# Kernel tuning notes

Measured on AMD Instinct MI355X. Metric: run time of the kernel, lower is better.

The kernel has to match this reference:

```python
import jax, jax.numpy as jnp
import numpy as np

H = 16   # num_heads
A = 64   # attn_size
D = 1024 # dims
NEG = -1000000000.0


def setup_inputs() -> dict:
    key = jax.random.key(0)
    k1, k2, k3, k4 = jax.random.split(key, 4)
    B, S = 2, 2048
    qs = jax.random.normal(k1, (B, S, D), dtype=jnp.float32)
    mask = jax.random.randint(k2, (B, S), 0, 2, dtype=jnp.int32)
    Wqkv = jax.random.normal(k3, (D, 3 * H * A), dtype=jnp.float32) * (1.0 / np.sqrt(D))
    Wout = jax.random.normal(k4, (H * A, D), dtype=jnp.float32) * (1.0 / np.sqrt(H * A))
    bout = jnp.zeros((D,), dtype=jnp.float32)
    return {"qs": qs, "mask": mask, "Wqkv": Wqkv, "Wout": Wout, "bout": bout}


def reference(qs, mask, Wqkv, Wout, bout):
    B, S, _ = qs.shape
    qkv = qs @ Wqkv                              # [B,S,3*H*A]
    qkv = qkv.reshape(B, S, 3 * H, A)            # split axis=2 in thirds (TF layout)
    q = jnp.transpose(qkv[:, :, 0:H, :], (0, 2, 1, 3))        # [B,H,S,A]
    k = jnp.transpose(qkv[:, :, H:2 * H, :], (0, 2, 1, 3))    # [B,H,S,A]
    v = jnp.transpose(qkv[:, :, 2 * H:3 * H, :], (0, 2, 1, 3))# [B,H,S,A]
    scores = jnp.einsum('bhqa,bhka->bhqk', q, k) / jnp.sqrt(jnp.float32(A))
    m = mask[:, None, None, :]                   # [B,1,1,S] broadcast over heads, queries
    scores = jnp.where(m == 0, NEG, scores)
    probs = jax.nn.softmax(scores, axis=-1)      # dropout_prob=0 / inference -> identity
    ctx = jnp.einsum('bhqk,bhka->bhqa', probs, v)  # [B,H,S,A]
    ctx = jnp.transpose(ctx, (0, 2, 1, 3)).reshape(B, S, H * A)
    return ctx @ Wout + bout
```

## Files before the change

### kernel.cpp

```cpp
#include <hip/hip_runtime.h>
#include <stdint.h>


typedef unsigned short u16;
typedef uint32_t u32;
typedef u16   u16x4  __attribute__((ext_vector_type(4)));
typedef u16   u16x8  __attribute__((ext_vector_type(8)));
typedef __bf16 bf16x8 __attribute__((ext_vector_type(8)));
typedef float f32x4  __attribute__((ext_vector_type(4)));

#define DEV __device__ __forceinline__

DEV u16 cvt_bf(float f) {
    return __builtin_bit_cast(u16, (__bf16)f);
}

DEV void async16(const void* g, void* l) {
    __builtin_amdgcn_global_load_lds(
        reinterpret_cast<const uint32_t __attribute__((address_space(1)))*>(
            reinterpret_cast<uintptr_t>(g)),
        reinterpret_cast<uint32_t __attribute__((address_space(3)))*>(
            reinterpret_cast<uintptr_t>(l)),
        16, 0, 0);
}

DEV f32x4 mfma16(bf16x8 a, bf16x8 b, f32x4 c) {
    return __builtin_amdgcn_mfma_f32_16x16x32_bf16(a, b, c, 0, 0, 0);
}


__global__ void k_prep(const float* __restrict__ qs, u16* __restrict__ qs_bf,
                       const int* __restrict__ m, float* __restrict__ bias) {
    int bid = blockIdx.x;
    if (bid < 4096) {
        int i = (bid * 256 + threadIdx.x) * 4;
        float4 v = *reinterpret_cast<const float4*>(qs + i);
        u16x4 o = { cvt_bf(v.x), cvt_bf(v.y), cvt_bf(v.z), cvt_bf(v.w) };
        *reinterpret_cast<u16x4*>(qs_bf + i) = o;
    } else {
        int i = (bid - 4096) * 256 + threadIdx.x;
        bias[i] = m[i] ? 0.0f : -1.0e9f;
    }
}

__global__ void k_tconv(const float* __restrict__ Wqkv, u16* __restrict__ WqkvT,
                        const float* __restrict__ Wout, u16* __restrict__ WoutT) {
    __shared__ float t[32][33];
    int bid = blockIdx.x;
    const float* src; u16* dst; int R, C, bx, by;
    if (bid < 3072) { src = Wqkv; dst = WqkvT; R = 1024; C = 3072; bx = bid % 96; by = bid / 96; }
    else { bid -= 3072; src = Wout; dst = WoutT; R = 1024; C = 1024; bx = bid % 32; by = bid / 32; }
    int c0 = bx * 32, r0 = by * 32;
    int tx = threadIdx.x & 31, ty = threadIdx.x >> 5;
#pragma unroll
    for (int i = 0; i < 4; ++i)
        t[ty + 8 * i][tx] = src[(size_t)(r0 + ty + 8 * i) * C + c0 + tx];
    __syncthreads();
#pragma unroll
    for (int i = 0; i < 4; ++i)
        dst[(size_t)(c0 + ty + 8 * i) * R + r0 + tx] = cvt_bf(t[tx][ty + 8 * i]);
}


template <int BM, bool OUT_BF16, bool HAS_BIAS>
__global__ __launch_bounds__(512, 4) void k_gemm(
    const u16* __restrict__ A, const u16* __restrict__ Bt,
    void* __restrict__ Cv, const float* __restrict__ bias,
    int M, int N, int K)
{
    constexpr int MT = BM / 32;
    __shared__ __attribute__((aligned(16))) u16 As[2][BM * 32];
    __shared__ __attribute__((aligned(16))) u16 Bs[2][128 * 32];

    const int tid = threadIdx.x, wave = tid >> 6, lane = tid & 63;
    const int lh = lane & 15, lg = lane >> 4;
    const int nbn = N >> 7;

    const int nwg = gridDim.x;
    const int q8 = nwg >> 3, r8 = nwg & 7;
    const int xcd = blockIdx.x & 7, li = blockIdx.x >> 3;
    const int wg = (xcd < r8 ? xcd * (q8 + 1) : r8 * (q8 + 1) + (xcd - r8) * q8) + li;

    const int m0 = (wg / nbn) * BM, n0 = (wg % nbn) * 128;
    const int wm = wave >> 2, wn = wave & 3;
    const int nk = K >> 5;

    const int srow = tid >> 2, scc = tid & 3;
    const int ssc = scc ^ (srow & 3);

    auto stage = [&](int buf, int kt) {
        if (tid < BM * 4)
            async16(A + (size_t)(m0 + srow) * K + kt * 32 + ssc * 8, &As[buf][tid * 8]);
        async16(Bt + (size_t)(n0 + srow) * K + kt * 32 + ssc * 8, &Bs[buf][tid * 8]);
    };

    f32x4 acc[MT][2] = {};
    stage(0, 0);
    for (int kt = 0; kt < nk; ++kt) {
        __syncthreads();
        if (kt + 1 < nk) stage((kt + 1) & 1, kt + 1);
        const int buf = kt & 1;
        bf16x8 af[MT], bf_[2];
#pragma unroll
        for (int mt = 0; mt < MT; ++mt) {
            int row = wm * (BM / 2) + mt * 16 + lh;
            int off = row * 32 + ((lg ^ (row & 3)) * 8);
            af[mt] = __builtin_bit_cast(bf16x8,
                     *reinterpret_cast<const u16x8*>(&As[buf][off]));
        }
#pragma unroll
        for (int nt = 0; nt < 2; ++nt) {
            int row = wn * 32 + nt * 16 + lh;
            int off = row * 32 + ((lg ^ (row & 3)) * 8);
            bf_[nt] = __builtin_bit_cast(bf16x8,
                      *reinterpret_cast<const u16x8*>(&Bs[buf][off]));
        }
        __builtin_amdgcn_s_setprio(1);
#pragma unroll
        for (int mt = 0; mt < MT; ++mt)
#pragma unroll
            for (int nt = 0; nt < 2; ++nt)
                acc[mt][nt] = mfma16(af[mt], bf_[nt], acc[mt][nt]);
        __builtin_amdgcn_s_setprio(0);
        __syncthreads();
    }

#pragma unroll
    for (int mt = 0; mt < MT; ++mt)
#pragma unroll
        for (int nt = 0; nt < 2; ++nt) {
            int col = n0 + wn * 32 + nt * 16 + lh;
#pragma unroll
            for (int r = 0; r < 4; ++r) {
                int row = m0 + wm * (BM / 2) + mt * 16 + 4 * lg + r;
                float v = acc[mt][nt][r];
                if (HAS_BIAS) v += bias[col];
                if (OUT_BF16) ((u16*)Cv)[(size_t)row * N + col] = cvt_bf(v);
                else          ((float*)Cv)[(size_t)row * N + col] = v;
            }
        }
}


__global__ __launch_bounds__(512, 4) void k_attn(
    const u16* __restrict__ qkv, const float* __restrict__ biasg, u16* __restrict__ ctx)
{
    __shared__ __attribute__((aligned(16))) u16 Ks[2][64 * 64];
    __shared__ __attribute__((aligned(16))) u16 Vt[2][64 * 72];
    __shared__ __attribute__((aligned(16))) u16 Ps[8 * 16 * 72];

    const int tid = threadIdx.x, wave = tid >> 6, lane = tid & 63;
    const int lh = lane & 15, lg = lane >> 4;

    const int wg = (blockIdx.x & 7) * 64 + (blockIdx.x >> 3);
    const int qt = wg & 15, bh = wg >> 4;
    const int b = bh >> 4, h = bh & 15;

    const u16* qbase = qkv + ((size_t)b * 2048 * 48 + h) * 64;
    const u16* kbase = qkv + ((size_t)b * 2048 * 48 + 16 + h) * 64;
    const u16* vbase = qkv + ((size_t)b * 2048 * 48 + 32 + h) * 64;
    const float* brow = biasg + b * 2048;

    const int srow = wave * 8 + (lane >> 3);
    const int scc  = lane & 7;
    const int ksrc = scc ^ (srow & 7);
    const int vswz = srow ^ (scc << 3);

    bf16x8 qf[2];
    {
        int row = qt * 128 + wave * 16 + lh;
        qf[0] = __builtin_bit_cast(bf16x8,
            *reinterpret_cast<const u16x8*>(qbase + (size_t)row * 3072 + lg * 8));
        qf[1] = __builtin_bit_cast(bf16x8,
            *reinterpret_cast<const u16x8*>(qbase + (size_t)row * 3072 + 32 + lg * 8));
    }

    f32x4 oa[4] = {};
    float lst[4] = {0.0f, 0.0f, 0.0f, 0.0f};

    u16* Pw = &Ps[wave * 16 * 72];

    {
        async16(kbase + (size_t)srow * 3072 + ksrc * 8, &Ks[0][wave * 512]);
        u16x8 v = *reinterpret_cast<const u16x8*>(vbase + (size_t)srow * 3072 + scc * 8);
#pragma unroll
        for (int j = 0; j < 8; ++j) Vt[0][(scc * 8 + j) * 72 + vswz] = v[j];
    }

    for (int kt = 0; kt < 32; ++kt) {
        __syncthreads();
        const int buf = kt & 1;
        if (kt + 1 < 32) {
            async16(kbase + (size_t)((kt + 1) * 64 + srow) * 3072 + ksrc * 8, &Ks[buf ^ 1][wave * 512]);
            u16x8 v = *reinterpret_cast<const u16x8*>(
                vbase + (size_t)((kt + 1) * 64 + srow) * 3072 + scc * 8);
#pragma unroll
            for (int j = 0; j < 8; ++j) Vt[buf ^ 1][(scc * 8 + j) * 72 + vswz] = v[j];
        }

        float biasv[4];
#pragma unroll
        for (int nt = 0; nt < 4; ++nt) biasv[nt] = brow[kt * 64 + nt * 16 + lh];

        f32x4 sa[4] = {};
        __builtin_amdgcn_s_setprio(1);
#pragma unroll
        for (int ks = 0; ks < 2; ++ks) {
            bf16x8 kb[4];
#pragma unroll
            for (int nt = 0; nt < 4; ++nt) {
                int row = nt * 16 + lh;
                int off = row * 64 + (((ks * 4 + lg) ^ (row & 7)) << 3);
                kb[nt] = __builtin_bit_cast(bf16x8,
                         *reinterpret_cast<const u16x8*>(&Ks[buf][off]));
            }
#pragma unroll
            for (int nt = 0; nt < 4; ++nt)
                sa[nt] = mfma16(qf[ks], kb[nt], sa[nt]);
        }
        __builtin_amdgcn_s_setprio(0);

#pragma unroll
        for (int nt = 0; nt < 4; ++nt)
#pragma unroll
            for (int r = 0; r < 4; ++r) {
                float e = __expf(fmaf(sa[nt][r], 0.125f, biasv[nt]));
                lst[r] += e;
                Pw[(4 * lg + r) * 72 + nt * 16 + lh] = cvt_bf(e);
            }

        __builtin_amdgcn_s_setprio(1);
#pragma unroll
        for (int ks = 0; ks < 2; ++ks) {
            bf16x8 pa = __builtin_bit_cast(bf16x8,
                        *reinterpret_cast<const u16x8*>(Pw + lh * 72 + ks * 32 + lg * 8));
            bf16x8 vb[4];
#pragma unroll
            for (int nt = 0; nt < 4; ++nt) {
                int col = nt * 16 + lh;
                int g = (col >> 3) & 7;
                int off = col * 72 + (((ks * 4 + lg) ^ g) << 3);
                vb[nt] = __builtin_bit_cast(bf16x8,
                         *reinterpret_cast<const u16x8*>(&Vt[buf][off]));
            }
#pragma unroll
            for (int nt = 0; nt < 4; ++nt)
                oa[nt] = mfma16(pa, vb[nt], oa[nt]);
        }
        __builtin_amdgcn_s_setprio(0);
    }

#pragma unroll
    for (int r = 0; r < 4; ++r) {
        float s = lst[r];
#pragma unroll
        for (int o = 1; o < 16; o <<= 1) s += __shfl_xor(s, o);
        lst[r] = 1.0f / s;
    }

#pragma unroll
    for (int nt = 0; nt < 4; ++nt)
#pragma unroll
        for (int r = 0; r < 4; ++r) {
            int row = qt * 128 + wave * 16 + 4 * lg + r;
            ctx[(size_t)(b * 2048 + row) * 1024 + h * 64 + nt * 16 + lh] = cvt_bf(oa[nt][r] * lst[r]);
        }
}


extern "C" void kernel_launch(void* const* d_in, const int* in_sizes, int n_in,
                              void* d_out, int out_size, void* d_ws, size_t ws_size,
                              hipStream_t stream)
{
    const float* qs   = (const float*)d_in[0];
    const int*   mask = (const int*)d_in[1];
    const float* Wqkv = (const float*)d_in[2];
    const float* Wout = (const float*)d_in[3];
    const float* bout = (const float*)d_in[4];
    float* out = (float*)d_out;

    char* ws = (char*)d_ws;
    u16*   qs_bf = (u16*)(ws);
    u16*   WqkvT = (u16*)(ws + 8388608);
    u16*   WoutT = (u16*)(ws + 14680064);
    u16*   qkvb  = (u16*)(ws + 16777216);
    u16*   ctxb  = (u16*)(ws + 41943040);
    float* biasb = (float*)(ws + 50331648);

    k_prep<<<4112, 256, 0, stream>>>(qs, qs_bf, mask, biasb);
    k_tconv<<<4096, 256, 0, stream>>>(Wqkv, WqkvT, Wout, WoutT);

    k_gemm<128, true, false><<<768, 512, 0, stream>>>(qs_bf, WqkvT, qkvb, nullptr, 4096, 3072, 1024);
    k_attn<<<512, 512, 0, stream>>>(qkvb, biasb, ctxb);
    k_gemm<64, false, true><<<512, 512, 0, stream>>>(ctxb, WoutT, out, bout, 4096, 1024, 1024);
}
```

Before: 194.3 us.

## Merge prep and transpose kernels; retile GEMMs to 4-wave blocks with larger per-wave tiles

Folds the weight transpose/convert kernel into the prep kernel so one launch covers the input cast, mask bias and both weight transposes. The GEMM moves from 8 waves of 512 threads to 4 waves of 256 threads in a 2x2 layout. Each wave now computes a larger output tile (more MFMAs per fragment load), and a BN template parameter is added. The output GEMM switches from a 64x128 to a 128x64 tile and the double-buffer indexing is reorganised. This trades fewer waves per block and higher register pressure for better operand reuse and one fewer launch.

```diff
diff --git a/kernel.cpp b/kernel.cpp
--- a/kernel.cpp
+++ b/kernel.cpp
@@ -30,26 +30,26 @@
 
 
 __global__ void k_prep(const float* __restrict__ qs, u16* __restrict__ qs_bf,
-                       const int* __restrict__ m, float* __restrict__ bias) {
+                       const int* __restrict__ m, float* __restrict__ bias,
+                       const float* __restrict__ Wqkv, u16* __restrict__ WqkvT,
+                       const float* __restrict__ Wout, u16* __restrict__ WoutT) {
+    __shared__ float t[32][33];
     int bid = blockIdx.x;
     if (bid < 4096) {
         int i = (bid * 256 + threadIdx.x) * 4;
         float4 v = *reinterpret_cast<const float4*>(qs + i);
         u16x4 o = { cvt_bf(v.x), cvt_bf(v.y), cvt_bf(v.z), cvt_bf(v.w) };
         *reinterpret_cast<u16x4*>(qs_bf + i) = o;
-    } else {
+        return;
+    }
+    if (bid < 4112) {
         int i = (bid - 4096) * 256 + threadIdx.x;
         bias[i] = m[i] ? 0.0f : -1.0e9f;
-    }
-}
-
-__global__ void k_tconv(const float* __restrict__ Wqkv, u16* __restrict__ WqkvT,
-                        const float* __restrict__ Wout, u16* __restrict__ WoutT) {
-    __shared__ float t[32][33];
-    int bid = blockIdx.x;
+        return;
+    }
     const float* src; u16* dst; int R, C, bx, by;
-    if (bid < 3072) { src = Wqkv; dst = WqkvT; R = 1024; C = 3072; bx = bid % 96; by = bid / 96; }
-    else { bid -= 3072; src = Wout; dst = WoutT; R = 1024; C = 1024; bx = bid % 32; by = bid / 32; }
+    if (bid < 7184) { int q = bid - 4112; src = Wqkv; dst = WqkvT; R = 1024; C = 3072; bx = q % 96; by = q / 96; }
+    else            { int q = bid - 7184; src = Wout; dst = WoutT; R = 1024; C = 1024; bx = q % 32; by = q / 32; }
     int c0 = bx * 32, r0 = by * 32;
     int tx = threadIdx.x & 31, ty = threadIdx.x >> 5;
 #pragma unroll
@@ -62,45 +62,53 @@
 }
 
 
-template <int BM, bool OUT_BF16, bool HAS_BIAS>
-__global__ __launch_bounds__(512, 4) void k_gemm(
+template <int BM, int BN, bool OUT_BF16, bool HAS_BIAS>
+__global__ __launch_bounds__(256, 3) void k_gemm(
     const u16* __restrict__ A, const u16* __restrict__ Bt,
     void* __restrict__ Cv, const float* __restrict__ bias,
     int M, int N, int K)
 {
-    constexpr int MT = BM / 32;
+    constexpr int MT = BM / 32, NT = BN / 32;
     __shared__ __attribute__((aligned(16))) u16 As[2][BM * 32];
-    __shared__ __attribute__((aligned(16))) u16 Bs[2][128 * 32];
+    __shared__ __attribute__((aligned(16))) u16 Bs[2][BN * 32];
 
     const int tid = threadIdx.x, wave = tid >> 6, lane = tid & 63;
     const int lh = lane & 15, lg = lane >> 4;
-    const int nbn = N >> 7;
+    const int nbn = N / BN;
 
     const int nwg = gridDim.x;
     const int q8 = nwg >> 3, r8 = nwg & 7;
     const int xcd = blockIdx.x & 7, li = blockIdx.x >> 3;
     const int wg = (xcd < r8 ? xcd * (q8 + 1) : r8 * (q8 + 1) + (xcd - r8) * q8) + li;
 
-    const int m0 = (wg / nbn) * BM, n0 = (wg % nbn) * 128;
-    const int wm = wave >> 2, wn = wave & 3;
+    const int m0 = (wg / nbn) * BM, n0 = (wg % nbn) * BN;
+    const int wm = wave >> 1, wn = wave & 1;
     const int nk = K >> 5;
 
-    const int srow = tid >> 2, scc = tid & 3;
-    const int ssc = scc ^ (srow & 3);
-
     auto stage = [&](int buf, int kt) {
-        if (tid < BM * 4)
-            async16(A + (size_t)(m0 + srow) * K + kt * 32 + ssc * 8, &As[buf][tid * 8]);
-        async16(Bt + (size_t)(n0 + srow) * K + kt * 32 + ssc * 8, &Bs[buf][tid * 8]);
+#pragma unroll
+        for (int i = 0; i < BM / 64; ++i) {
+            int c = i * 256 + tid;
+            int row = c >> 2, cc = c & 3;
+            int sc = cc ^ (row & 3);
+            async16(A + (size_t)(m0 + row) * K + kt * 32 + sc * 8, &As[buf][c * 8]);
+        }
+#pragma unroll
+        for (int i = 0; i < BN / 64; ++i) {
+            int c = i * 256 + tid;
+            int row = c >> 2, cc = c & 3;
+            int sc = cc ^ (row & 3);
+            async16(Bt + (size_t)(n0 + row) * K + kt * 32 + sc * 8, &Bs[buf][c * 8]);
+        }
     };
 
-    f32x4 acc[MT][2] = {};
+    f32x4 acc[MT][NT] = {};
     stage(0, 0);
+    __syncthreads();
+    int buf = 0;
     for (int kt = 0; kt < nk; ++kt) {
-        __syncthreads();
-        if (kt + 1 < nk) stage((kt + 1) & 1, kt + 1);
-        const int buf = kt & 1;
-        bf16x8 af[MT], bf_[2];
+        if (kt + 1 < nk) stage(buf ^ 1, kt + 1);
+        bf16x8 af[MT], bf_[NT];
 #pragma unroll
         for (int mt = 0; mt < MT; ++mt) {
             int row = wm * (BM / 2) + mt * 16 + lh;
@@ -109,8 +117,8 @@
                      *reinterpret_cast<const u16x8*>(&As[buf][off]));
         }
 #pragma unroll
-        for (int nt = 0; nt < 2; ++nt) {
-            int row = wn * 32 + nt * 16 + lh;
+        for (int nt = 0; nt < NT; ++nt) {
+            int row = wn * (BN / 2) + nt * 16 + lh;
             int off = row * 32 + ((lg ^ (row & 3)) * 8);
             bf_[nt] = __builtin_bit_cast(bf16x8,
                       *reinterpret_cast<const u16x8*>(&Bs[buf][off]));
@@ -119,17 +127,18 @@
 #pragma unroll
         for (int mt = 0; mt < MT; ++mt)
 #pragma unroll
-            for (int nt = 0; nt < 2; ++nt)
+            for (int nt = 0; nt < NT; ++nt)
                 acc[mt][nt] = mfma16(af[mt], bf_[nt], acc[mt][nt]);
         __builtin_amdgcn_s_setprio(0);
         __syncthreads();
+        buf ^= 1;
     }
 
 #pragma unroll
     for (int mt = 0; mt < MT; ++mt)
 #pragma unroll
-        for (int nt = 0; nt < 2; ++nt) {
-            int col = n0 + wn * 32 + nt * 16 + lh;
+        for (int nt = 0; nt < NT; ++nt) {
+            int col = n0 + wn * (BN / 2) + nt * 16 + lh;
 #pragma unroll
             for (int r = 0; r < 4; ++r) {
                 int row = m0 + wm * (BM / 2) + mt * 16 + 4 * lg + r;
@@ -287,10 +296,9 @@
     u16*   ctxb  = (u16*)(ws + 41943040);
     float* biasb = (float*)(ws + 50331648);
 
-    k_prep<<<4112, 256, 0, stream>>>(qs, qs_bf, mask, biasb);
-    k_tconv<<<4096, 256, 0, stream>>>(Wqkv, WqkvT, Wout, WoutT);
-
-    k_gemm<128, true, false><<<768, 512, 0, stream>>>(qs_bf, WqkvT, qkvb, nullptr, 4096, 3072, 1024);
+    k_prep<<<8208, 256, 0, stream>>>(qs, qs_bf, mask, biasb, Wqkv, WqkvT, Wout, WoutT);
+
+    k_gemm<128, 128, true, false><<<768, 256, 0, stream>>>(qs_bf, WqkvT, qkvb, nullptr, 4096, 3072, 1024);
     k_attn<<<512, 512, 0, stream>>>(qkvb, biasb, ctxb);
-    k_gemm<64, false, true><<<512, 512, 0, stream>>>(ctxb, WoutT, out, bout, 4096, 1024, 1024);
-}
+    k_gemm<128, 64, false, true><<<512, 256, 0, stream>>>(ctxb, WoutT, out, bout, 4096, 1024, 1024);
+}
```

Result: no change. 193.5 us (-0.4%).
